# Optimization experiments

Hardware: AMD Instinct MI355X
Metric: run time of the kernel (lower is better)

Reference implementation:

```python
import jax, jax.numpy as jnp
import numpy as np

# ---- static config (matches init_kwargs) ----
IM_W, IM_H = 1280.0, 720.0
HAND_D, OBJ_D, JOINT_D = 0.05, 0.05, 0.05
NUM_OBJ_CLASSES = 42
G = NUM_OBJ_CLASSES - 2  # num_good_obj_classes = 40
TOP_K = 1
N_JOINTS = 22
T = 25000
# delta vector layout: [rh_x, rh_y, lh_x, lh_y, obj_x, obj_y, joint_x, joint_y]
RHX, RHY, LHX, LHY, OX, OY, JX, JY = range(8)
DELTA_BOUNDS = np.array([IM_W * HAND_D, IM_H * HAND_D, IM_W * HAND_D, IM_H * HAND_D,
                         IM_W * OBJ_D, IM_H * OBJ_D, IM_W * JOINT_D, IM_H * JOINT_D],
                        dtype=np.float32)


def _build_layout():
    """Replay the sequential `ind` walk once to build per-feature static tables:
    mod  [D] bool  : whether this slot gets offset+clamp
    lim  [D] float : clamp upper bound (im_w for x, im_h for y)
    coef [D,8]     : coefficients applied to the 8 per-frame deltas
    All option flags are True for this feat_version.
    """
    mods, lims, coefs = [], [], []

    def skip(n=1):
        for _ in range(n):
            mods.append(False); lims.append(1.0); coefs.append(np.zeros(8, np.float32))

    def mod(lim, *delta_idxs):
        c = np.zeros(8, np.float32)
        for d in delta_idxs:
            c[d] = 1.0
        mods.append(True); lims.append(lim); coefs.append(c)

    for _k in range(TOP_K):
        skip()                                    # right hand activation
        for _ in range(G):                        # obj <-> right hand dists
            mod(IM_W, RHX, OX); mod(IM_H, RHY, OY)
        mod(IM_W, RHX); mod(IM_H, RHY)            # rh image-center dist
        skip()                                    # left hand activation
        for _ in range(G):                        # obj <-> left hand dists
            mod(IM_W, LHX, OX); mod(IM_H, LHY, OY)
        mod(IM_W, LHX); mod(IM_H, LHY)            # lh image-center dist
        mod(IM_W, RHX, LHX); mod(IM_H, RHY, LHY)  # rh <-> lh dist
        skip()                                    # rh/lh intersection
        for _ in range(G):
            skip(1)                               # obj activation
            skip(2)                               # intersections
            mod(IM_W, OX); mod(IM_H, OY)          # obj image-center dist
    # joint-hand offsets
    for _ in range(N_JOINTS):
        mod(IM_W, LHX, JX); mod(IM_H, LHY, JY)
    for _ in range(N_JOINTS):
        mod(IM_W, RHX, JX); mod(IM_H, RHY, JY)
    # joint-object offsets
    for _k in range(TOP_K):
        for _ in range(G):
            for _ in range(N_JOINTS):
                mod(IM_W, OX, JX); mod(IM_H, OY, JY)

    return (np.array(mods), np.array(lims, np.float32), np.stack(coefs))


_MOD, _LIM, _COEF = _build_layout()   # D = 2217
D = _MOD.shape[0]
assert D == 2217
MOD = jnp.asarray(_MOD)
LIM = jnp.asarray(_LIM)
COEF = jnp.asarray(_COEF)             # [D, 8]


def setup_inputs() -> dict:
    key = jax.random.key(0)
    k1, k2 = jax.random.split(key)
    features = jax.random.uniform(k1, (T, D), dtype=jnp.float32) * IM_W
    # per-frame deltas uniform in +-bound, matching init_deltas()
    deltas = (jax.random.uniform(k2, (T, 8), dtype=jnp.float32) * 2.0 - 1.0) \
             * jnp.asarray(DELTA_BOUNDS)
    return {"features": features, "deltas": deltas}


def reference(features, deltas):
    # offset per (frame, feature): [T,8] @ [8,D] -> [T,D]
    offset = deltas @ COEF.T
    shifted = jnp.clip(features + offset, 0.0, LIM)
    # modified slots: x != 0 -> clamp(x+off); x == 0 stays 0 (clamp(0)=0)
    out = jnp.where(MOD & (features != 0), shifted, features)
    return out
```

## Files before the change

kernel.cpp:

```cpp
#include <hip/hip_runtime.h>
#include <hip/hip_bf16.h>
#include <stdint.h>


#define D_FEAT 2217u

__global__ void build_meta_kernel(uint32_t* __restrict__ meta) {
    int d = blockIdx.x * blockDim.x + threadIdx.x;
    if (d >= (int)D_FEAT) return;

    int a = 0, b = 0;
    bool mod = true, hasB = false;

    if (d == 0 || d == 83 || d == 168) {
        mod = false;
    } else if (d <= 80) {
        int o = d - 1;
        if ((o & 1) == 0) { a = 0; b = 4; } else { a = 1; b = 5; }
        hasB = true;
    } else if (d == 81) { a = 0;
    } else if (d == 82) { a = 1;
    } else if (d <= 163) {
        int o = d - 84;
        if ((o & 1) == 0) { a = 2; b = 4; } else { a = 3; b = 5; }
        hasB = true;
    } else if (d == 164) { a = 2;
    } else if (d == 165) { a = 3;
    } else if (d == 166) { a = 0; b = 2; hasB = true;
    } else if (d == 167) { a = 1; b = 3; hasB = true;
    } else if (d <= 368) {
        int o = (d - 169) % 5;
        if (o < 3) { mod = false; }
        else if (o == 3) { a = 4; }
        else { a = 5; }
    } else if (d <= 412) {
        int o = d - 369;
        if ((o & 1) == 0) { a = 2; b = 6; } else { a = 3; b = 7; }
        hasB = true;
    } else if (d <= 456) {
        int o = d - 413;
        if ((o & 1) == 0) { a = 0; b = 6; } else { a = 1; b = 7; }
        hasB = true;
    } else {
        int o = d - 457;
        if ((o & 1) == 0) { a = 4; b = 6; } else { a = 5; b = 7; }
        hasB = true;
    }

    uint32_t limH = (uint32_t)(a & 1);
    uint32_t pack = (mod ? 1u : 0u) | (hasB ? 2u : 0u) | (limH << 2)
                  | ((uint32_t)a << 3) | ((uint32_t)b << 6);
    meta[d] = pack;
}

__global__ __launch_bounds__(256) void move_center_pts_kernel(
    const float* __restrict__ feat,
    const float* __restrict__ deltas,
    const uint32_t* __restrict__ meta,
    float* __restrict__ out,
    unsigned n4) {
    unsigned stride = gridDim.x * blockDim.x;
    for (unsigned i4 = blockIdx.x * blockDim.x + threadIdx.x; i4 < n4; i4 += stride) {
        unsigned base = i4 * 4u;
        unsigned t = base / D_FEAT;
        unsigned d = base - t * D_FEAT;
        unsigned t8 = t * 8u;

        const float4 f4 = reinterpret_cast<const float4*>(feat)[i4];
        float fv[4] = {f4.x, f4.y, f4.z, f4.w};
        float ov[4];

        #pragma unroll
        for (int j = 0; j < 4; ++j) {
            uint32_t p = meta[d];
            float dA = deltas[t8 + ((p >> 3) & 7u)];
            float dB = deltas[t8 + ((p >> 6) & 7u)];
            float off = dA + ((p & 2u) ? dB : 0.0f);
            float lim = (p & 4u) ? 720.0f : 1280.0f;
            float f = fv[j];
            float s = fminf(fmaxf(f + off, 0.0f), lim);
            ov[j] = ((p & 1u) && (f != 0.0f)) ? s : f;
            ++d;
            if (d == D_FEAT) { d = 0u; t8 += 8u; }
        }

        float4 o4;
        o4.x = ov[0]; o4.y = ov[1]; o4.z = ov[2]; o4.w = ov[3];
        reinterpret_cast<float4*>(out)[i4] = o4;
    }
}

extern "C" void kernel_launch(void* const* d_in, const int* in_sizes, int n_in,
                              void* d_out, int out_size, void* d_ws, size_t ws_size,
                              hipStream_t stream) {
    const float* feat   = (const float*)d_in[0];
    const float* deltas = (const float*)d_in[1];
    float* out = (float*)d_out;
    uint32_t* meta = (uint32_t*)d_ws;

    build_meta_kernel<<<(D_FEAT + 255) / 256, 256, 0, stream>>>(meta);

    unsigned total = (unsigned)in_sizes[0];
    unsigned n4 = total / 4u;
    unsigned blocks = (n4 + 255u) / 256u;
    if (blocks > 2048u) blocks = 2048u;
    move_center_pts_kernel<<<blocks, 256, 0, stream>>>(feat, deltas, meta, out, n4);
}
```

Measured before the change: 385.8 us.

## Assign one block per frame row with specialized joint-object fast path

Replaces the grid-stride flat loop with one 192-thread block per frame. Each block handles misaligned head and tail elements individually and processes the aligned middle with vector loads. For the large joint-object region (index 457 onward), the per-element meta lookup and gathered delta loads are replaced by two precomputed offsets and limits chosen by parity. This removes per-element integer division and meta/delta memory traffic, but launches 25000 small blocks that each do about three loop iterations per thread.

```diff
diff --git a/kernel.cpp b/kernel.cpp
--- a/kernel.cpp
+++ b/kernel.cpp
@@ -4,6 +4,7 @@
 
 
 #define D_FEAT 2217u
+typedef float f32x4 __attribute__((ext_vector_type(4)));
 
 __global__ void build_meta_kernel(uint32_t* __restrict__ meta) {
     int d = blockIdx.x * blockDim.x + threadIdx.x;
@@ -53,40 +54,69 @@
     meta[d] = pack;
 }
 
-__global__ __launch_bounds__(256) void move_center_pts_kernel(
+__device__ __forceinline__ float xform_meta(float f, uint32_t p,
+                                            const float* __restrict__ dl) {
+    float dA = dl[(p >> 3) & 7u];
+    float dB = dl[(p >> 6) & 7u];
+    float off = dA + ((p & 2u) ? dB : 0.0f);
+    float lim = (p & 4u) ? 720.0f : 1280.0f;
+    float s = fminf(fmaxf(f + off, 0.0f), lim);
+    return ((p & 1u) && (f != 0.0f)) ? s : f;
+}
+
+__global__ __launch_bounds__(192) void move_center_pts_kernel(
     const float* __restrict__ feat,
     const float* __restrict__ deltas,
     const uint32_t* __restrict__ meta,
-    float* __restrict__ out,
-    unsigned n4) {
-    unsigned stride = gridDim.x * blockDim.x;
-    for (unsigned i4 = blockIdx.x * blockDim.x + threadIdx.x; i4 < n4; i4 += stride) {
-        unsigned base = i4 * 4u;
-        unsigned t = base / D_FEAT;
-        unsigned d = base - t * D_FEAT;
-        unsigned t8 = t * 8u;
+    float* __restrict__ out) {
+    unsigned r = blockIdx.x;
+    size_t base = (size_t)r * D_FEAT;
+    const float* dl = deltas + (size_t)r * 8u;
 
-        const float4 f4 = reinterpret_cast<const float4*>(feat)[i4];
-        float fv[4] = {f4.x, f4.y, f4.z, f4.w};
-        float ov[4];
+    float offx = dl[4] + dl[6];
+    float offy = dl[5] + dl[7];
 
-        #pragma unroll
-        for (int j = 0; j < 4; ++j) {
-            uint32_t p = meta[d];
-            float dA = deltas[t8 + ((p >> 3) & 7u)];
-            float dB = deltas[t8 + ((p >> 6) & 7u)];
-            float off = dA + ((p & 2u) ? dB : 0.0f);
-            float lim = (p & 4u) ? 720.0f : 1280.0f;
-            float f = fv[j];
-            float s = fminf(fmaxf(f + off, 0.0f), lim);
-            ov[j] = ((p & 1u) && (f != 0.0f)) ? s : f;
-            ++d;
-            if (d == D_FEAT) { d = 0u; t8 += 8u; }
+    unsigned align_off = (unsigned)((4u - ((unsigned)base & 3u)) & 3u);
+    size_t a0 = base + align_off;
+    unsigned L = D_FEAT - align_off;
+    unsigned ngroups = L >> 2;
+    unsigned tail_rem = L & 3u;
+    unsigned tid = threadIdx.x;
+
+    if (tid < align_off) {
+        float f = feat[base + tid];
+        out[base + tid] = xform_meta(f, meta[tid], dl);
+    }
+    if (tid < tail_rem) {
+        unsigned d = align_off + (ngroups << 2) + tid;
+        float f = feat[base + d];
+        out[base + d] = xform_meta(f, meta[d], dl);
+    }
+
+    bool odd0 = (align_off & 1u) != 0u;
+    float offA = odd0 ? offx : offy, limA = odd0 ? 1280.0f : 720.0f;
+    float offB = odd0 ? offy : offx, limB = odd0 ? 720.0f : 1280.0f;
+
+    const f32x4* f4p = reinterpret_cast<const f32x4*>(feat + a0);
+    f32x4* o4p = reinterpret_cast<f32x4*>(out + a0);
+
+    for (unsigned g = tid; g < ngroups; g += 192u) {
+        unsigned d0 = align_off + (g << 2);
+        f32x4 f4 = f4p[g];
+        f32x4 o4;
+        if (d0 >= 457u) {
+            float f, s;
+            f = f4.x; s = fminf(fmaxf(f + offA, 0.0f), limA); o4.x = (f != 0.0f) ? s : f;
+            f = f4.y; s = fminf(fmaxf(f + offB, 0.0f), limB); o4.y = (f != 0.0f) ? s : f;
+            f = f4.z; s = fminf(fmaxf(f + offA, 0.0f), limA); o4.z = (f != 0.0f) ? s : f;
+            f = f4.w; s = fminf(fmaxf(f + offB, 0.0f), limB); o4.w = (f != 0.0f) ? s : f;
+        } else {
+            o4.x = xform_meta(f4.x, meta[d0 + 0u], dl);
+            o4.y = xform_meta(f4.y, meta[d0 + 1u], dl);
+            o4.z = xform_meta(f4.z, meta[d0 + 2u], dl);
+            o4.w = xform_meta(f4.w, meta[d0 + 3u], dl);
         }
-
-        float4 o4;
-        o4.x = ov[0]; o4.y = ov[1]; o4.z = ov[2]; o4.w = ov[3];
-        reinterpret_cast<float4*>(out)[i4] = o4;
+        o4p[g] = o4;
     }
 }
 
@@ -100,9 +130,6 @@
 
     build_meta_kernel<<<(D_FEAT + 255) / 256, 256, 0, stream>>>(meta);
 
-    unsigned total = (unsigned)in_sizes[0];
-    unsigned n4 = total / 4u;
-    unsigned blocks = (n4 + 255u) / 256u;
-    if (blocks > 2048u) blocks = 2048u;
-    move_center_pts_kernel<<<blocks, 256, 0, stream>>>(feat, deltas, meta, out, n4);
+    unsigned T = (unsigned)(in_sizes[0] / (int)D_FEAT);
+    move_center_pts_kernel<<<T, 192, 0, stream>>>(feat, deltas, meta, out);
 }
```

Result: faster. 373.4 us (-3.2%).
